# Optimization experiments

Hardware: AMD Instinct MI355X
Metric: run time of the kernel (lower is better)

## Reference

```python
import jax, jax.numpy as jnp
import numpy as np

B, S, D, F, E, K = 4, 2048, 1024, 2048, 8, 2


def setup_inputs() -> dict:
    key = jax.random.key(0)
    ks = jax.random.split(key, 6)
    s_in = 1.0 / np.sqrt(D)
    s_ff = 1.0 / np.sqrt(F)
    return {
        "x": jax.random.normal(ks[0], (B, S, D), jnp.float32),
        "rms_w": jnp.ones((D,), jnp.float32),
        "Wg": jax.random.normal(ks[1], (D, E), jnp.float32) * s_in,
        "bg": jnp.zeros((E,), jnp.float32),
        "W1a": jax.random.normal(ks[2], (E, D, F), jnp.float32) * s_in,
        "b1a": jnp.zeros((E, F), jnp.float32),
        "W1b": jax.random.normal(ks[3], (E, D, F), jnp.float32) * s_in,
        "b1b": jnp.zeros((E, F), jnp.float32),
        "W2": jax.random.normal(ks[4], (E, F, D), jnp.float32) * s_ff,
        "b2": jnp.zeros((E, D), jnp.float32),
    }


def reference(x, rms_w, Wg, bg, W1a, b1a, W1b, b1b, W2, b2):
    # RMSNorm (torch nn.RMSNorm with eps=None -> finfo eps)
    eps = jnp.finfo(x.dtype).eps
    x = x * jax.lax.rsqrt(jnp.mean(x * x, axis=-1, keepdims=True) + eps) * rms_w

    # top-k gating
    logits = x @ Wg + bg                              # [B,S,E]
    topk_vals, topk_idx = jax.lax.top_k(logits, K)    # [B,S,K]
    topk_w = jax.nn.softmax(topk_vals, axis=-1)       # [B,S,K]
    one_hot = jax.nn.one_hot(topk_idx, E, dtype=x.dtype)  # [B,S,K,E]
    weights = jnp.sum(one_hot * topk_w[..., None], axis=2)  # [B,S,E]

    # dense per-expert SwiGLU (faithful to the masked dense loop)
    a = jnp.einsum("bsd,edf->bsef", x, W1a) + b1a     # [B,S,E,F]
    b = jnp.einsum("bsd,edf->bsef", x, W1b) + b1b
    h = jax.nn.silu(a) * b
    y = jnp.einsum("bsef,efd->bsed", h, W2) + b2      # [B,S,E,D]
    out = jnp.einsum("bse,bsed->bsd", weights, y)     # [B,S,D]
    return out, weights
```

## Files before the change

### kernel.cpp

```cpp
#include <hip/hip_runtime.h>
#include <hip/hip_bf16.h>

#define DD 1024
#define FF 2048
#define EE 8
#define NT 8192
#define NRCAP 17280
#define MAXT128 135

typedef __attribute__((ext_vector_type(8))) short bf16x8;
typedef __attribute__((ext_vector_type(4))) float f32x4;

__device__ __forceinline__ ushort f2bf(float f) {
  __hip_bfloat16 h = __float2bfloat16(f);
  return *reinterpret_cast<ushort*>(&h);
}

__device__ __forceinline__ void gload16(const void* g, void* l) {
  __builtin_amdgcn_global_load_lds((const __attribute__((address_space(1))) void*)g,
                                   (__attribute__((address_space(3))) void*)l, 16, 0, 0);
}

__device__ __forceinline__ int swz_of_row(int r) { return ((r >> 1) & 3) << 4; }

__global__ __launch_bounds__(256) void k_transpose64(const float* __restrict__ in,
                                                     ushort* __restrict__ outT, int R, int C) {
  __shared__ ushort tile[64][68];
  const int e = blockIdx.z;
  const int c0 = blockIdx.x * 64, r0 = blockIdx.y * 64;
  const float* ip = in + (size_t)e * R * C;
  const int cq = threadIdx.x & 15, rr = threadIdx.x >> 4;
  #pragma unroll
  for (int p = 0; p < 4; p++) {
    const int r = rr + 16 * p;
    float4 v = *reinterpret_cast<const float4*>(ip + (size_t)(r0 + r) * C + c0 + 4 * cq);
    ushort4 u = make_ushort4(f2bf(v.x), f2bf(v.y), f2bf(v.z), f2bf(v.w));
    *reinterpret_cast<ushort4*>(&tile[r][4 * cq]) = u;
  }
  __syncthreads();
  ushort* op = outT + (size_t)e * C * R;
  const int rq = threadIdx.x & 15, cc = threadIdx.x >> 4;
  #pragma unroll
  for (int p = 0; p < 4; p++) {
    const int c = cc + 16 * p;
    ushort4 u = make_ushort4(tile[4 * rq + 0][c], tile[4 * rq + 1][c],
                             tile[4 * rq + 2][c], tile[4 * rq + 3][c]);
    *reinterpret_cast<ushort4*>(op + (size_t)(c0 + c) * R + r0 + 4 * rq) = u;
  }
}

__global__ __launch_bounds__(256) void k_transpose_pair64(const float* __restrict__ in,
                                                          ushort* __restrict__ outT, int half) {
  __shared__ ushort tile[64][68];
  const int e = blockIdx.z;
  const int f0 = blockIdx.x * 64, d0 = blockIdx.y * 64;
  const float* ip = in + (size_t)e * DD * FF;
  const int cq = threadIdx.x & 15, rr = threadIdx.x >> 4;
  #pragma unroll
  for (int p = 0; p < 4; p++) {
    const int r = rr + 16 * p;
    float4 v = *reinterpret_cast<const float4*>(ip + (size_t)(d0 + r) * FF + f0 + 4 * cq);
    ushort4 u = make_ushort4(f2bf(v.x), f2bf(v.y), f2bf(v.z), f2bf(v.w));
    *reinterpret_cast<ushort4*>(&tile[r][4 * cq]) = u;
  }
  __syncthreads();
  ushort* op = outT + (size_t)e * 4096 * DD;
  const int rq = threadIdx.x & 15, cc = threadIdx.x >> 4;
  #pragma unroll
  for (int p = 0; p < 4; p++) {
    const int f = f0 + cc + 16 * p;
    const int rmap = ((f >> 4) << 5) + half * 16 + (f & 15);
    ushort4 u = make_ushort4(tile[4 * rq + 0][cc + 16 * p], tile[4 * rq + 1][cc + 16 * p],
                             tile[4 * rq + 2][cc + 16 * p], tile[4 * rq + 3][cc + 16 * p]);
    *reinterpret_cast<ushort4*>(op + (size_t)rmap * DD + d0 + 4 * rq) = u;
  }
}

__global__ __launch_bounds__(256) void k_rms_gate(
    const float* __restrict__ x, const float* __restrict__ rms_w,
    const float* __restrict__ Wg, const float* __restrict__ bg,
    ushort* __restrict__ xn, float* __restrict__ outW,
    int* __restrict__ tk_e, float* __restrict__ tk_w) {
  const int t = blockIdx.x * 4 + (threadIdx.x >> 6);
  const int lane = threadIdx.x & 63;
  const float* xrow = x + (size_t)t * DD;
  const float4* x4 = reinterpret_cast<const float4*>(xrow);
  const float4* w4 = reinterpret_cast<const float4*>(rms_w);
  const float4* Wg4 = reinterpret_cast<const float4*>(Wg);
  float4 xv[4];
  float ss = 0.f;
  #pragma unroll
  for (int i = 0; i < 4; i++) {
    xv[i] = x4[i * 64 + lane];
    ss += xv[i].x * xv[i].x + xv[i].y * xv[i].y + xv[i].z * xv[i].z + xv[i].w * xv[i].w;
  }
  #pragma unroll
  for (int m = 32; m; m >>= 1) ss += __shfl_xor(ss, m);
  const float sc = 1.0f / sqrtf(ss * (1.0f / (float)DD) + 1.1920929e-07f);
  ushort4* xout = reinterpret_cast<ushort4*>(xn + (size_t)t * DD);
  #pragma unroll
  for (int i = 0; i < 4; i++) {
    const float4 wv = w4[i * 64 + lane];
    xout[i * 64 + lane] = make_ushort4(f2bf(xv[i].x * sc * wv.x), f2bf(xv[i].y * sc * wv.y),
                                       f2bf(xv[i].z * sc * wv.z), f2bf(xv[i].w * sc * wv.w));
  }
  float4 lgv = make_float4(0.f, 0.f, 0.f, 0.f);
  #pragma unroll 8
  for (int k = 0; k < 32; k++) {
    const int d = (lane >> 1) + 32 * k;
    const float s = xrow[d] * sc * rms_w[d];
    const float4 wg = Wg4[lane + 64 * k];
    lgv.x += s * wg.x; lgv.y += s * wg.y; lgv.z += s * wg.z; lgv.w += s * wg.w;
  }
  #pragma unroll
  for (int m = 32; m >= 2; m >>= 1) {
    lgv.x += __shfl_xor(lgv.x, m);
    lgv.y += __shfl_xor(lgv.y, m);
    lgv.z += __shfl_xor(lgv.z, m);
    lgv.w += __shfl_xor(lgv.w, m);
  }
  float4 other;
  other.x = __shfl(lgv.x, lane ^ 1);
  other.y = __shfl(lgv.y, lane ^ 1);
  other.z = __shfl(lgv.z, lane ^ 1);
  other.w = __shfl(lgv.w, lane ^ 1);
  if (lane == 0) {
    float l[8] = { lgv.x + bg[0], lgv.y + bg[1], lgv.z + bg[2], lgv.w + bg[3],
                   other.x + bg[4], other.y + bg[5], other.z + bg[6], other.w + bg[7] };
    int i0 = 0; float v0 = l[0];
    #pragma unroll
    for (int i = 1; i < 8; i++) if (l[i] > v0) { v0 = l[i]; i0 = i; }
    int i1 = -1; float v1 = -3.4e38f;
    #pragma unroll
    for (int i = 0; i < 8; i++) if (i != i0 && l[i] > v1) { v1 = l[i]; i1 = i; }
    const float e1v = __expf(v1 - v0);
    const float w0 = 1.0f / (1.0f + e1v);
    const float w1 = e1v * w0;
    float wout[8] = {0.f, 0.f, 0.f, 0.f, 0.f, 0.f, 0.f, 0.f};
    wout[i0] = w0; wout[i1] = w1;
    float4* wrow = reinterpret_cast<float4*>(outW + (size_t)t * EE);
    wrow[0] = make_float4(wout[0], wout[1], wout[2], wout[3]);
    wrow[1] = make_float4(wout[4], wout[5], wout[6], wout[7]);
    tk_e[t] = i0 | (i1 << 8);
    tk_w[2 * t] = w0; tk_w[2 * t + 1] = w1;
  }
}

__global__ void k_scan(const int* __restrict__ tk_e, int* __restrict__ base,
                       int* __restrict__ tok_of_row) {
  const int tid = threadIdx.x, wid = tid >> 6, lane = tid & 63;
  int c[8] = {0, 0, 0, 0, 0, 0, 0, 0};
  for (int i = tid; i < NT; i += 256) {
    const int ee = tk_e[i];
    c[ee & 255]++;
    c[(ee >> 8) & 255]++;
  }
  #pragma unroll
  for (int m = 32; m; m >>= 1) {
    #pragma unroll
    for (int i = 0; i < 8; i++) c[i] += __shfl_xor(c[i], m);
  }
  __shared__ int sw[4][8];
  if (lane == 0) {
    #pragma unroll
    for (int i = 0; i < 8; i++) sw[wid][i] = c[i];
  }
  __syncthreads();
  if (tid == 0) {
    int acc = 0;
    for (int e = 0; e < EE; e++) {
      base[e] = acc;
      const int cnt = sw[0][e] + sw[1][e] + sw[2][e] + sw[3][e];
      acc += ((cnt + 127) >> 7) << 7;
    }
    base[EE] = acc;
  }
  for (int i = tid; i < NRCAP; i += 256) tok_of_row[i] = -1;
}

__global__ __launch_bounds__(256) void k_scatter(
    const int* __restrict__ tk_e, const int* __restrict__ base,
    int* __restrict__ tok_of_row, int* __restrict__ rows_of_tok) {
  const int e = blockIdx.x;
  const int tid = threadIdx.x, wid = tid >> 6, lane = tid & 63;
  __shared__ int s_cursor;
  __shared__ int s_woff[4];
  if (tid == 0) s_cursor = base[e];
  __syncthreads();
  for (int t0 = 0; t0 < NT; t0 += 256) {
    const int t = t0 + tid;
    const int ee = tk_e[t];
    const int m0 = (ee & 255) == e;
    const int m1 = ((ee >> 8) & 255) == e;
    const int has = m0 | m1;
    const unsigned long long mask = __ballot(has);
    const int prefix = __popcll(mask & ((1ull << lane) - 1ull));
    if (lane == 0) s_woff[wid] = __popcll(mask);
    __syncthreads();
    int woff = 0;
    #pragma unroll
    for (int w = 0; w < 4; w++) woff += (w < wid) ? s_woff[w] : 0;
    if (has) {
      const int row = s_cursor + woff + prefix;
      tok_of_row[row] = t;
      rows_of_tok[2 * t + (m0 ? 0 : 1)] = row;
    }
    __syncthreads();
    if (tid == 0) s_cursor += s_woff[0] + s_woff[1] + s_woff[2] + s_woff[3];
  }
}

__global__ __launch_bounds__(256) void k_ffn1(
    const ushort* __restrict__ xn, const ushort* __restrict__ BT1,
    const float* __restrict__ b1a, const float* __restrict__ b1b,
    const int* __restrict__ tok_of_row, const int* __restrict__ base,
    ushort* __restrict__ H) {
  const int row0 = blockIdx.y * 128;
  if (row0 >= base[EE]) return;
  int e = 0;
  while (e < EE - 1 && row0 >= base[e + 1]) e++;
  const int c0 = blockIdx.x * 128;
  const int tid = threadIdx.x, wid = tid >> 6, lane = tid & 63;
  const int wr = wid >> 1, wc = wid & 1;
  __shared__ __align__(16) ushort smem[128 * 72];
  ushort* sA = smem;
  ushort* sB = smem + 4096;
  const int rloc = tid >> 2;
  const int kcol = (((tid & 3) * 16) ^ swz_of_row(rloc)) >> 1;
  int tok0 = tok_of_row[row0 + rloc];      if (tok0 < 0) tok0 = 0;
  int tok1 = tok_of_row[row0 + 64 + rloc]; if (tok1 < 0) tok1 = 0;
  const ushort* gA0 = xn + (size_t)tok0 * DD + kcol;
  const ushort* gA1 = xn + (size_t)tok1 * DD + kcol;
  const ushort* gB0 = BT1 + ((size_t)e * 4096 + c0 + rloc) * DD + kcol;
  const ushort* gB1 = BT1 + ((size_t)e * 4096 + c0 + 64 + rloc) * DD + kcol;
  ushort* lA0 = sA + wid * 512;  ushort* lA1 = sA + 2048 + wid * 512;
  ushort* lB0 = sB + wid * 512;  ushort* lB1 = sB + 2048 + wid * 512;
  const int lrow = lane & 15, q = lane >> 4;
  const int fsw = (q * 16) ^ swz_of_row(lrow);
  int aoff[4], boff[4];
  #pragma unroll
  for (int m = 0; m < 4; m++) aoff[m] = (wr * 64 + m * 16 + lrow) * 64 + fsw;
  #pragma unroll
  for (int n = 0; n < 4; n++) boff[n] = (wc * 64 + n * 16 + lrow) * 64 + fsw;
  f32x4 acc[16];
  #pragma unroll
  for (int i = 0; i < 16; i++) acc[i] = (f32x4){0.f, 0.f, 0.f, 0.f};
  for (int kt = 0; kt < DD / 32; kt++) {
    gload16(gA0 + kt * 32, lA0);
    gload16(gA1 + kt * 32, lA1);
    gload16(gB0 + kt * 32, lB0);
    gload16(gB1 + kt * 32, lB1);
    __syncthreads();
    bf16x8 fb[4];
    #pragma unroll
    for (int n = 0; n < 4; n++)
      fb[n] = *reinterpret_cast<const bf16x8*>(reinterpret_cast<const char*>(sB) + boff[n]);
    #pragma unroll
    for (int m = 0; m < 4; m++) {
      const bf16x8 fa = *reinterpret_cast<const bf16x8*>(reinterpret_cast<const char*>(sA) + aoff[m]);
      #pragma unroll
      for (int n = 0; n < 4; n++)
        acc[m * 4 + n] = __builtin_amdgcn_mfma_f32_16x16x32_bf16(fa, fb[n], acc[m * 4 + n], 0, 0, 0);
    }
    __syncthreads();
  }
  #pragma unroll
  for (int np = 0; np < 2; np++) {
    const int fl = wc * 32 + np * 16 + lrow;
    const int f = (c0 >> 1) + fl;
    const float ba_ = b1a[e * FF + f], bb_ = b1b[e * FF + f];
    #pragma unroll
    for (int m = 0; m < 4; m++) {
      #pragma unroll
      for (int r = 0; r < 4; r++) {
        const float a = acc[m * 4 + 2 * np][r] + ba_;
        const float b = acc[m * 4 + 2 * np + 1][r] + bb_;
        const float h = (a / (1.0f + __expf(-a))) * b;
        const int rl = wr * 64 + m * 16 + q * 4 + r;
        smem[rl * 72 + fl] = f2bf(h);
      }
    }
  }
  __syncthreads();
  const int fc = tid & 7, rb = tid >> 3;
  #pragma unroll
  for (int i = 0; i < 4; i++) {
    const int rl = i * 32 + rb;
    const uint4 v = *reinterpret_cast<const uint4*>(&smem[rl * 72 + fc * 8]);
    *reinterpret_cast<uint4*>(H + (size_t)(row0 + rl) * FF + (c0 >> 1) + fc * 8) = v;
  }
}

__global__ __launch_bounds__(256) void k_ffn2(
    const ushort* __restrict__ H, const ushort* __restrict__ W2T, const float* __restrict__ b2,
    const int* __restrict__ base, float* __restrict__ Y) {
  const int row0 = blockIdx.y * 128;
  if (row0 >= base[EE]) return;
  int e = 0;
  while (e < EE - 1 && row0 >= base[e + 1]) e++;
  const int d0 = blockIdx.x * 128;
  const int tid = threadIdx.x, wid = tid >> 6, lane = tid & 63;
  const int wr = wid >> 1, wc = wid & 1;
  __shared__ ushort sA[128 * 32], sB[128 * 32];
  const int rloc = tid >> 2;
  const int kcol = (((tid & 3) * 16) ^ swz_of_row(rloc)) >> 1;
  const ushort* gA0 = H + (size_t)(row0 + rloc) * FF + kcol;
  const ushort* gA1 = H + (size_t)(row0 + 64 + rloc) * FF + kcol;
  const ushort* gB0 = W2T + ((size_t)e * DD + d0 + rloc) * FF + kcol;
  const ushort* gB1 = W2T + ((size_t)e * DD + d0 + 64 + rloc) * FF + kcol;
  ushort* lA0 = sA + wid * 512;  ushort* lA1 = sA + 2048 + wid * 512;
  ushort* lB0 = sB + wid * 512;  ushort* lB1 = sB + 2048 + wid * 512;
  const int lrow = lane & 15, q = lane >> 4;
  const int fsw = (q * 16) ^ swz_of_row(lrow);
  int aoff[4], boff[4];
  #pragma unroll
  for (int m = 0; m < 4; m++) aoff[m] = (wr * 64 + m * 16 + lrow) * 64 + fsw;
  #pragma unroll
  for (int n = 0; n < 4; n++) boff[n] = (wc * 64 + n * 16 + lrow) * 64 + fsw;
  f32x4 acc[16];
  #pragma unroll
  for (int i = 0; i < 16; i++) acc[i] = (f32x4){0.f, 0.f, 0.f, 0.f};
  for (int kt = 0; kt < FF / 32; kt++) {
    gload16(gA0 + kt * 32, lA0);
    gload16(gA1 + kt * 32, lA1);
    gload16(gB0 + kt * 32, lB0);
    gload16(gB1 + kt * 32, lB1);
    __syncthreads();
    bf16x8 fb[4];
    #pragma unroll
    for (int n = 0; n < 4; n++)
      fb[n] = *reinterpret_cast<const bf16x8*>(reinterpret_cast<const char*>(sB) + boff[n]);
    #pragma unroll
    for (int m = 0; m < 4; m++) {
      const bf16x8 fa = *reinterpret_cast<const bf16x8*>(reinterpret_cast<const char*>(sA) + aoff[m]);
      #pragma unroll
      for (int n = 0; n < 4; n++)
        acc[m * 4 + n] = __builtin_amdgcn_mfma_f32_16x16x32_bf16(fa, fb[n], acc[m * 4 + n], 0, 0, 0);
    }
    __syncthreads();
  }
  #pragma unroll
  for (int n = 0; n < 4; n++) {
    const int dcol = d0 + wc * 64 + n * 16 + lrow;
    const float bias = b2[e * DD + dcol];
    #pragma unroll
    for (int m = 0; m < 4; m++) {
      #pragma unroll
      for (int r = 0; r < 4; r++) {
        const int grow = row0 + wr * 64 + m * 16 + q * 4 + r;
        Y[(size_t)grow * DD + dcol] = acc[m * 4 + n][r] + bias;
      }
    }
  }
}

__global__ __launch_bounds__(256) void k_gather(
    const float* __restrict__ Y, const int* __restrict__ rows_of_tok,
    const float* __restrict__ tk_w, float* __restrict__ out0) {
  for (int t = blockIdx.x; t < NT; t += gridDim.x) {
    const int r0 = rows_of_tok[2 * t], r1 = rows_of_tok[2 * t + 1];
    const float w0 = tk_w[2 * t], w1 = tk_w[2 * t + 1];
    const float4 y0 = reinterpret_cast<const float4*>(Y + (size_t)r0 * DD)[threadIdx.x];
    const float4 y1 = reinterpret_cast<const float4*>(Y + (size_t)r1 * DD)[threadIdx.x];
    float4 o;
    o.x = w0 * y0.x + w1 * y1.x;
    o.y = w0 * y0.y + w1 * y1.y;
    o.z = w0 * y0.z + w1 * y1.z;
    o.w = w0 * y0.w + w1 * y1.w;
    reinterpret_cast<float4*>(out0 + (size_t)t * DD)[threadIdx.x] = o;
  }
}

#define WS_Y    ((size_t)0)
#define WS_XN   ((size_t)0)
#define WS_BT1  ((size_t)16777216)
#define WS_W2T  ((size_t)83886080)
#define WS_H    ((size_t)117440512)
#define WS_TOK  ((size_t)188219392)
#define WS_ROWS ((size_t)188288512)
#define WS_TKE  ((size_t)188354048)
#define WS_TKW  ((size_t)188386816)
#define WS_BASE ((size_t)188452352)

extern "C" void kernel_launch(void* const* d_in, const int* in_sizes, int n_in,
                              void* d_out, int out_size, void* d_ws, size_t ws_size,
                              hipStream_t stream) {
  const float* x     = (const float*)d_in[0];
  const float* rms_w = (const float*)d_in[1];
  const float* Wg    = (const float*)d_in[2];
  const float* bg    = (const float*)d_in[3];
  const float* W1a   = (const float*)d_in[4];
  const float* b1a   = (const float*)d_in[5];
  const float* W1b   = (const float*)d_in[6];
  const float* b1b   = (const float*)d_in[7];
  const float* W2    = (const float*)d_in[8];
  const float* b2    = (const float*)d_in[9];
  float* out0 = (float*)d_out;
  float* outW = (float*)d_out + (size_t)NT * DD;

  char* ws = (char*)d_ws;
  ushort* xn    = (ushort*)(ws + WS_XN);
  ushort* BT1   = (ushort*)(ws + WS_BT1);
  ushort* W2T   = (ushort*)(ws + WS_W2T);
  ushort* Hbuf  = (ushort*)(ws + WS_H);
  float*  Ybuf  = (float*)(ws + WS_Y);
  int*    tok   = (int*)(ws + WS_TOK);
  int*    rows  = (int*)(ws + WS_ROWS);
  int*    tk_e  = (int*)(ws + WS_TKE);
  float*  tk_w  = (float*)(ws + WS_TKW);
  int*    base  = (int*)(ws + WS_BASE);

  k_transpose_pair64<<<dim3(FF / 64, DD / 64, EE), 256, 0, stream>>>(W1a, BT1, 0);
  k_transpose_pair64<<<dim3(FF / 64, DD / 64, EE), 256, 0, stream>>>(W1b, BT1, 1);
  k_transpose64<<<dim3(DD / 64, FF / 64, EE), 256, 0, stream>>>(W2, W2T, FF, DD);

  k_rms_gate<<<NT / 4, 256, 0, stream>>>(x, rms_w, Wg, bg, xn, outW, tk_e, tk_w);
  k_scan<<<1, 256, 0, stream>>>(tk_e, base, tok);
  k_scatter<<<EE, 256, 0, stream>>>(tk_e, base, tok, rows);

  k_ffn1<<<dim3(4096 / 128, MAXT128), 256, 0, stream>>>(xn, BT1, b1a, b1b, tok, base, Hbuf);
  k_ffn2<<<dim3(DD / 128, MAXT128), 256, 0, stream>>>(Hbuf, W2T, b2, base, Ybuf);
  k_gather<<<2048, 256, 0, stream>>>(Ybuf, rows, tk_w, out0);
}
```

Measured before the change: 411.7 us.

## Fuse gather into FFN2 epilogue with atomics, merge transposes and scan

The three weight-transpose launches become one launch, and the scan kernel is folded into the per-expert scatter kernel, which recomputes the counts in every block. The separate gather pass and its fp32 Y buffer are removed: FFN2 now scales each row by its gate weight and atomically adds into the output, which the RMS kernel zeroes beforehand. This saves Y write/read traffic and several launches, but adds many scalar fp32 atomics with scattered addresses and makes the floating-point summation order nondeterministic.

```diff
diff --git a/kernel.cpp b/kernel.cpp
--- a/kernel.cpp
+++ b/kernel.cpp
@@ -23,63 +23,63 @@
 
 __device__ __forceinline__ int swz_of_row(int r) { return ((r >> 1) & 3) << 4; }
 
-__global__ __launch_bounds__(256) void k_transpose64(const float* __restrict__ in,
-                                                     ushort* __restrict__ outT, int R, int C) {
+__global__ __launch_bounds__(256) void k_transpose_all(
+    const float* __restrict__ W1a, const float* __restrict__ W1b,
+    const float* __restrict__ W2, ushort* __restrict__ BT1, ushort* __restrict__ W2T) {
   __shared__ ushort tile[64][68];
-  const int e = blockIdx.z;
-  const int c0 = blockIdx.x * 64, r0 = blockIdx.y * 64;
-  const float* ip = in + (size_t)e * R * C;
+  const int z = blockIdx.z;
   const int cq = threadIdx.x & 15, rr = threadIdx.x >> 4;
-  #pragma unroll
-  for (int p = 0; p < 4; p++) {
-    const int r = rr + 16 * p;
-    float4 v = *reinterpret_cast<const float4*>(ip + (size_t)(r0 + r) * C + c0 + 4 * cq);
-    ushort4 u = make_ushort4(f2bf(v.x), f2bf(v.y), f2bf(v.z), f2bf(v.w));
-    *reinterpret_cast<ushort4*>(&tile[r][4 * cq]) = u;
-  }
-  __syncthreads();
-  ushort* op = outT + (size_t)e * C * R;
-  const int rq = threadIdx.x & 15, cc = threadIdx.x >> 4;
-  #pragma unroll
-  for (int p = 0; p < 4; p++) {
-    const int c = cc + 16 * p;
-    ushort4 u = make_ushort4(tile[4 * rq + 0][c], tile[4 * rq + 1][c],
-                             tile[4 * rq + 2][c], tile[4 * rq + 3][c]);
-    *reinterpret_cast<ushort4*>(op + (size_t)(c0 + c) * R + r0 + 4 * rq) = u;
-  }
-}
-
-__global__ __launch_bounds__(256) void k_transpose_pair64(const float* __restrict__ in,
-                                                          ushort* __restrict__ outT, int half) {
-  __shared__ ushort tile[64][68];
-  const int e = blockIdx.z;
-  const int f0 = blockIdx.x * 64, d0 = blockIdx.y * 64;
-  const float* ip = in + (size_t)e * DD * FF;
-  const int cq = threadIdx.x & 15, rr = threadIdx.x >> 4;
-  #pragma unroll
-  for (int p = 0; p < 4; p++) {
-    const int r = rr + 16 * p;
-    float4 v = *reinterpret_cast<const float4*>(ip + (size_t)(d0 + r) * FF + f0 + 4 * cq);
-    ushort4 u = make_ushort4(f2bf(v.x), f2bf(v.y), f2bf(v.z), f2bf(v.w));
-    *reinterpret_cast<ushort4*>(&tile[r][4 * cq]) = u;
-  }
-  __syncthreads();
-  ushort* op = outT + (size_t)e * 4096 * DD;
-  const int rq = threadIdx.x & 15, cc = threadIdx.x >> 4;
-  #pragma unroll
-  for (int p = 0; p < 4; p++) {
-    const int f = f0 + cc + 16 * p;
-    const int rmap = ((f >> 4) << 5) + half * 16 + (f & 15);
-    ushort4 u = make_ushort4(tile[4 * rq + 0][cc + 16 * p], tile[4 * rq + 1][cc + 16 * p],
-                             tile[4 * rq + 2][cc + 16 * p], tile[4 * rq + 3][cc + 16 * p]);
-    *reinterpret_cast<ushort4*>(op + (size_t)rmap * DD + d0 + 4 * rq) = u;
+  if (z < 16) {
+    const int half = z >> 3, e = z & 7;
+    const float* ip = (half ? W1b : W1a) + (size_t)e * DD * FF;
+    const int f0 = blockIdx.x * 64, d0 = blockIdx.y * 64;
+    #pragma unroll
+    for (int p = 0; p < 4; p++) {
+      const int r = rr + 16 * p;
+      float4 v = *reinterpret_cast<const float4*>(ip + (size_t)(d0 + r) * FF + f0 + 4 * cq);
+      *reinterpret_cast<ushort4*>(&tile[r][4 * cq]) =
+          make_ushort4(f2bf(v.x), f2bf(v.y), f2bf(v.z), f2bf(v.w));
+    }
+    __syncthreads();
+    ushort* op = BT1 + (size_t)e * 4096 * DD;
+    const int rq = threadIdx.x & 15, cc = threadIdx.x >> 4;
+    #pragma unroll
+    for (int p = 0; p < 4; p++) {
+      const int f = f0 + cc + 16 * p;
+      const int rmap = ((f >> 4) << 5) + half * 16 + (f & 15);
+      ushort4 u = make_ushort4(tile[4 * rq + 0][cc + 16 * p], tile[4 * rq + 1][cc + 16 * p],
+                               tile[4 * rq + 2][cc + 16 * p], tile[4 * rq + 3][cc + 16 * p]);
+      *reinterpret_cast<ushort4*>(op + (size_t)rmap * DD + d0 + 4 * rq) = u;
+    }
+  } else {
+    const int e = z & 7;
+    const float* ip = W2 + (size_t)e * FF * DD;
+    const int r0 = blockIdx.x * 64;
+    const int c0 = blockIdx.y * 64;
+    #pragma unroll
+    for (int p = 0; p < 4; p++) {
+      const int r = rr + 16 * p;
+      float4 v = *reinterpret_cast<const float4*>(ip + (size_t)(r0 + r) * DD + c0 + 4 * cq);
+      *reinterpret_cast<ushort4*>(&tile[r][4 * cq]) =
+          make_ushort4(f2bf(v.x), f2bf(v.y), f2bf(v.z), f2bf(v.w));
+    }
+    __syncthreads();
+    ushort* op = W2T + (size_t)e * DD * FF;
+    const int rq = threadIdx.x & 15, cc = threadIdx.x >> 4;
+    #pragma unroll
+    for (int p = 0; p < 4; p++) {
+      const int c = cc + 16 * p;
+      ushort4 u = make_ushort4(tile[4 * rq + 0][c], tile[4 * rq + 1][c],
+                               tile[4 * rq + 2][c], tile[4 * rq + 3][c]);
+      *reinterpret_cast<ushort4*>(op + (size_t)(c0 + c) * FF + r0 + 4 * rq) = u;
+    }
   }
 }
 
 __global__ __launch_bounds__(256) void k_rms_gate(
     const float* __restrict__ x, const float* __restrict__ rms_w,
     const float* __restrict__ Wg, const float* __restrict__ bg,
-    ushort* __restrict__ xn, float* __restrict__ outW,
+    ushort* __restrict__ xn, float* __restrict__ out0, float* __restrict__ outW,
     int* __restrict__ tk_e, float* __restrict__ tk_w) {
   const int t = blockIdx.x * 4 + (threadIdx.x >> 6);
   const int lane = threadIdx.x & 63;
@@ -98,11 +98,13 @@
   for (int m = 32; m; m >>= 1) ss += __shfl_xor(ss, m);
   const float sc = 1.0f / sqrtf(ss * (1.0f / (float)DD) + 1.1920929e-07f);
   ushort4* xout = reinterpret_cast<ushort4*>(xn + (size_t)t * DD);
+  float4* orow = reinterpret_cast<float4*>(out0 + (size_t)t * DD);
   #pragma unroll
   for (int i = 0; i < 4; i++) {
     const float4 wv = w4[i * 64 + lane];
     xout[i * 64 + lane] = make_ushort4(f2bf(xv[i].x * sc * wv.x), f2bf(xv[i].y * sc * wv.y),
                                        f2bf(xv[i].z * sc * wv.z), f2bf(xv[i].w * sc * wv.w));
+    orow[i * 64 + lane] = make_float4(0.f, 0.f, 0.f, 0.f);
   }
   float4 lgv = make_float4(0.f, 0.f, 0.f, 0.f);
   #pragma unroll 8
@@ -146,8 +148,10 @@
   }
 }
 
-__global__ void k_scan(const int* __restrict__ tk_e, int* __restrict__ base,
-                       int* __restrict__ tok_of_row) {
+__global__ __launch_bounds__(256) void k_scatter(
+    const int* __restrict__ tk_e, const float* __restrict__ tk_w, int* __restrict__ base,
+    int* __restrict__ tok_of_row, float* __restrict__ gw_of_row) {
+  const int e = blockIdx.x;
   const int tid = threadIdx.x, wid = tid >> 6, lane = tid & 63;
   int c[8] = {0, 0, 0, 0, 0, 0, 0, 0};
   for (int i = tid; i < NT; i += 256) {
@@ -161,6 +165,7 @@
     for (int i = 0; i < 8; i++) c[i] += __shfl_xor(c[i], m);
   }
   __shared__ int sw[4][8];
+  __shared__ int s_base[9];
   if (lane == 0) {
     #pragma unroll
     for (int i = 0; i < 8; i++) sw[wid][i] = c[i];
@@ -168,24 +173,21 @@
   __syncthreads();
   if (tid == 0) {
     int acc = 0;
-    for (int e = 0; e < EE; e++) {
-      base[e] = acc;
-      const int cnt = sw[0][e] + sw[1][e] + sw[2][e] + sw[3][e];
+    for (int q = 0; q < EE; q++) {
+      s_base[q] = acc;
+      const int cnt = sw[0][q] + sw[1][q] + sw[2][q] + sw[3][q];
       acc += ((cnt + 127) >> 7) << 7;
     }
-    base[EE] = acc;
-  }
-  for (int i = tid; i < NRCAP; i += 256) tok_of_row[i] = -1;
-}
-
-__global__ __launch_bounds__(256) void k_scatter(
-    const int* __restrict__ tk_e, const int* __restrict__ base,
-    int* __restrict__ tok_of_row, int* __restrict__ rows_of_tok) {
-  const int e = blockIdx.x;
-  const int tid = threadIdx.x, wid = tid >> 6, lane = tid & 63;
+    s_base[EE] = acc;
+  }
+  __syncthreads();
+  if (e == 0 && tid <= EE) base[tid] = s_base[tid];
+  const int myBase = s_base[e], myEnd = s_base[e + 1];
+  for (int i = myBase + tid; i < myEnd; i += 256) tok_of_row[i] = -1;
+  __syncthreads();
   __shared__ int s_cursor;
   __shared__ int s_woff[4];
-  if (tid == 0) s_cursor = base[e];
+  if (tid == 0) s_cursor = myBase;
   __syncthreads();
   for (int t0 = 0; t0 < NT; t0 += 256) {
     const int t = t0 + tid;
@@ -203,7 +205,7 @@
     if (has) {
       const int row = s_cursor + woff + prefix;
       tok_of_row[row] = t;
-      rows_of_tok[2 * t + (m0 ? 0 : 1)] = row;
+      gw_of_row[row] = tk_w[2 * t + (m0 ? 0 : 1)];
     }
     __syncthreads();
     if (tid == 0) s_cursor += s_woff[0] + s_woff[1] + s_woff[2] + s_woff[3];
@@ -293,7 +295,8 @@
 
 __global__ __launch_bounds__(256) void k_ffn2(
     const ushort* __restrict__ H, const ushort* __restrict__ W2T, const float* __restrict__ b2,
-    const int* __restrict__ base, float* __restrict__ Y) {
+    const int* __restrict__ tok_of_row, const float* __restrict__ gw_of_row,
+    const int* __restrict__ base, float* __restrict__ out0) {
   const int row0 = blockIdx.y * 128;
   if (row0 >= base[EE]) return;
   int e = 0;
@@ -339,48 +342,38 @@
     }
     __syncthreads();
   }
+  int dcols[4]; float bias[4];
   #pragma unroll
   for (int n = 0; n < 4; n++) {
-    const int dcol = d0 + wc * 64 + n * 16 + lrow;
-    const float bias = b2[e * DD + dcol];
-    #pragma unroll
-    for (int m = 0; m < 4; m++) {
-      #pragma unroll
-      for (int r = 0; r < 4; r++) {
-        const int grow = row0 + wr * 64 + m * 16 + q * 4 + r;
-        Y[(size_t)grow * DD + dcol] = acc[m * 4 + n][r] + bias;
+    dcols[n] = d0 + wc * 64 + n * 16 + lrow;
+    bias[n] = b2[e * DD + dcols[n]];
+  }
+  #pragma unroll
+  for (int m = 0; m < 4; m++) {
+    #pragma unroll
+    for (int r = 0; r < 4; r++) {
+      const int grow = row0 + wr * 64 + m * 16 + q * 4 + r;
+      const int tk = tok_of_row[grow];
+      if (tk >= 0) {
+        const float gw = gw_of_row[grow];
+        float* orow = out0 + (size_t)tk * DD;
+        #pragma unroll
+        for (int n = 0; n < 4; n++)
+          atomicAdd(orow + dcols[n], gw * (acc[m * 4 + n][r] + bias[n]));
       }
     }
   }
 }
 
-__global__ __launch_bounds__(256) void k_gather(
-    const float* __restrict__ Y, const int* __restrict__ rows_of_tok,
-    const float* __restrict__ tk_w, float* __restrict__ out0) {
-  for (int t = blockIdx.x; t < NT; t += gridDim.x) {
-    const int r0 = rows_of_tok[2 * t], r1 = rows_of_tok[2 * t + 1];
-    const float w0 = tk_w[2 * t], w1 = tk_w[2 * t + 1];
-    const float4 y0 = reinterpret_cast<const float4*>(Y + (size_t)r0 * DD)[threadIdx.x];
-    const float4 y1 = reinterpret_cast<const float4*>(Y + (size_t)r1 * DD)[threadIdx.x];
-    float4 o;
-    o.x = w0 * y0.x + w1 * y1.x;
-    o.y = w0 * y0.y + w1 * y1.y;
-    o.z = w0 * y0.z + w1 * y1.z;
-    o.w = w0 * y0.w + w1 * y1.w;
-    reinterpret_cast<float4*>(out0 + (size_t)t * DD)[threadIdx.x] = o;
-  }
-}
-
-#define WS_Y    ((size_t)0)
 #define WS_XN   ((size_t)0)
 #define WS_BT1  ((size_t)16777216)
 #define WS_W2T  ((size_t)83886080)
 #define WS_H    ((size_t)117440512)
 #define WS_TOK  ((size_t)188219392)
-#define WS_ROWS ((size_t)188288512)
-#define WS_TKE  ((size_t)188354048)
-#define WS_TKW  ((size_t)188386816)
-#define WS_BASE ((size_t)188452352)
+#define WS_GW   ((size_t)188288512)
+#define WS_TKE  ((size_t)188357632)
+#define WS_TKW  ((size_t)188390400)
+#define WS_BASE ((size_t)188455936)
 
 extern "C" void kernel_launch(void* const* d_in, const int* in_sizes, int n_in,
                               void* d_out, int out_size, void* d_ws, size_t ws_size,
@@ -403,22 +396,17 @@
   ushort* BT1   = (ushort*)(ws + WS_BT1);
   ushort* W2T   = (ushort*)(ws + WS_W2T);
   ushort* Hbuf  = (ushort*)(ws + WS_H);
-  float*  Ybuf  = (float*)(ws + WS_Y);
   int*    tok   = (int*)(ws + WS_TOK);
-  int*    rows  = (int*)(ws + WS_ROWS);
+  float*  gw    = (float*)(ws + WS_GW);
   int*    tk_e  = (int*)(ws + WS_TKE);
   float*  tk_w  = (float*)(ws + WS_TKW);
   int*    base  = (int*)(ws + WS_BASE);
 
-  k_transpose_pair64<<<dim3(FF / 64, DD / 64, EE), 256, 0, stream>>>(W1a, BT1, 0);
-  k_transpose_pair64<<<dim3(FF / 64, DD / 64, EE), 256, 0, stream>>>(W1b, BT1, 1);
-  k_transpose64<<<dim3(DD / 64, FF / 64, EE), 256, 0, stream>>>(W2, W2T, FF, DD);
-
-  k_rms_gate<<<NT / 4, 256, 0, stream>>>(x, rms_w, Wg, bg, xn, outW, tk_e, tk_w);
-  k_scan<<<1, 256, 0, stream>>>(tk_e, base, tok);
-  k_scatter<<<EE, 256, 0, stream>>>(tk_e, base, tok, rows);
+  k_transpose_all<<<dim3(32, 16, 24), 256, 0, stream>>>(W1a, W1b, W2, BT1, W2T);
+
+  k_rms_gate<<<NT / 4, 256, 0, stream>>>(x, rms_w, Wg, bg, xn, out0, outW, tk_e, tk_w);
+  k_scatter<<<EE, 256, 0, stream>>>(tk_e, tk_w, base, tok, gw);
 
   k_ffn1<<<dim3(4096 / 128, MAXT128), 256, 0, stream>>>(xn, BT1, b1a, b1b, tok, base, Hbuf);
-  k_ffn2<<<dim3(DD / 128, MAXT128), 256, 0, stream>>>(Hbuf, W2T, b2, base, Ybuf);
-  k_gather<<<2048, 256, 0, stream>>>(Ybuf, rows, tk_w, out0);
-}
+  k_ffn2<<<dim3(DD / 128, MAXT128), 256, 0, stream>>>(Hbuf, W2T, b2, tok, gw, base, out0);
+}
```

After: 436.0 us. 5.9% more time.
